# Kernel optimization log

Hardware: AMD Instinct MI355X
Metric: run time of the kernel (lower is better)

## Reference

```python
import jax, jax.numpy as jnp
import numpy as np

RUNS, WAYS, SHOT, QUERIES, D = 512, 5, 5, 15, 640
NS, QS = WAYS * SHOT, WAYS * QUERIES
LAM, ALPHA, UPDATE_RATE, EPOCHS = 10.0, 0.7, 0.6, 3
OT_EPS, OT_MAXITERS = 1e-3, 1000


def compute_entropy(P):
    # P: (runs, n, ways); normalized entropy per row
    P = P + 1e-12
    P = P / P.sum(axis=2, keepdims=True)
    H = -jnp.sum(P * jnp.log(P), axis=2)
    return H / jnp.log(jnp.asarray(P.shape[2], P.dtype))


def sq_cdist(a, b):
    # squared euclidean distance, (runs,n,d) x (runs,m,d) -> (runs,n,m)
    d2 = (a * a).sum(-1)[:, :, None] + (b * b).sum(-1)[:, None, :] \
         - 2.0 * jnp.einsum('bnd,bmd->bnm', a, b)
    return jnp.maximum(d2, 0.0)


def get_distance(f1, f2):
    return jnp.exp(-LAM * sq_cdist(f1, f2))


def build_graph(W):
    n = W.shape[1]
    W = W * (1.0 - jnp.eye(n, dtype=W.dtype)[None])  # zero diagonal
    Dm = W.sum(-1) ** -0.5                            # D^{-1/2}
    return Dm[:, None, :] * W * Dm[:, :, None]


def sinkhorn(M, n_l, labels, eps):
    # faithful port of compute_optimal_transport (class_balance=True)
    nr, n, ways = M.shape
    r = jnp.ones((nr, n), M.dtype)
    c = jnp.full((nr, ways), float(n // ways), M.dtype)  # ones*n//ways (floor)
    onehot = jax.nn.one_hot(labels[:, :n_l], ways, dtype=M.dtype) if n_l > 0 else None

    def cond(st):
        P, u, it = st
        return (jnp.max(jnp.abs(u - P.sum(2))) > eps) & (it <= OT_MAXITERS)

    def body(st):
        P, u, it = st
        u = P.sum(2)
        P = P * (r / u)[:, :, None]
        P = P * (c / P.sum(1))[:, None, :]
        if n_l > 0:
            P = P.at[:, :n_l, :].set(onehot)  # fill_(0) + scatter_(2, labels, 1)
        return P, u, it + 1

    P, _, _ = jax.lax.while_loop(cond, body, (M, jnp.zeros((nr, n), M.dtype), jnp.int32(1)))
    return P


def get_prob(features, proto, ys):
    d2 = sq_cdist(features, proto)
    Pq = jnp.exp(-LAM * d2[:, NS:])
    Pq = sinkhorn(Pq, 0, ys, 1e-3)
    Ps = jax.nn.one_hot(ys, WAYS, dtype=d2.dtype)  # scatter on support rows
    return jnp.concatenate([Ps, Pq], axis=1)


def _forward(xs, xq, ys, yq):
    features = jnp.concatenate([xs, xq], axis=1)           # (runs, ns+qs, d)
    labels = jnp.concatenate([ys, yq], axis=1)
    runs = features.shape[0]
    proto = features[:, :NS].reshape(runs, WAYS, SHOT, -1).mean(axis=2)
    Z = None
    for _ in range(EPOCHS):  # (pre-loop Z / Inverse_W in torch code are dead code)
        features = features[:, :NS + QS]
        Z = get_prob(features, proto, ys)
        ent = compute_entropy(Z)
        Z = Z * (1.0 - ent[..., None])
        # update_prototype
        new_proto = jnp.einsum('bnk,bnd->bkd', Z, features) / Z.sum(axis=1)[..., None]
        proto = (1.0 - UPDATE_RATE) * proto + UPDATE_RATE * new_proto
        dist_proto = get_distance(proto, proto)
        score = compute_entropy(dist_proto)
        omega = ent.mean(axis=1, keepdims=True)
        mask = (score < omega).astype(Z.dtype)             # (runs, ways)
        add_proto = proto * mask[..., None]
        dist_proto = dist_proto * mask[..., None]
        features = jnp.concatenate([features, add_proto], axis=1)  # (runs, ns+qs+ways, d)
        Z = jnp.concatenate([Z, dist_proto], axis=1)
        dist = get_distance(features, features)
        W = build_graph(dist)
        n = features.shape[1]
        Inv = jnp.linalg.inv(jnp.eye(n, dtype=W.dtype)[None] - ALPHA * W)
        Z = Inv @ Z                                         # (I - aW)^{-1} diffusion
        Z = sinkhorn(Z, NS, ys, OT_EPS)
    olabels = jnp.argmax(Z[:, :NS + QS], axis=2)
    matches = (labels == olabels).astype(jnp.float32)
    return matches[:, NS:].mean(axis=1)                     # acc_test: (runs,)


def setup_inputs() -> dict:
    key = jax.random.key(0)
    k1, k2, k3 = jax.random.split(key, 3)
    scale = 0.04  # keeps exp(-lam*dist^2) in fp32 normal range
    xs = scale * jax.random.normal(k1, (RUNS, NS, D), dtype=jnp.float32)
    xq = scale * jax.random.normal(k2, (RUNS, QS, D), dtype=jnp.float32)
    # support labels must be class-block ordered (proto reshape assumes it)
    ys = jnp.tile(jnp.repeat(jnp.arange(WAYS, dtype=jnp.int32), SHOT)[None, :], (RUNS, 1))
    yq = jax.random.randint(k3, (RUNS, QS), 0, WAYS, dtype=jnp.int32)
    return {'xs': xs, 'xq': xq, 'ys': ys, 'yq': yq}


def reference(xs, xq, ys, yq):
    return _forward(xs, xq, ys, yq)
```

## Files before the change

### kernel.cpp

```cpp
#include <hip/hip_runtime.h>
#include <math.h>

#define RUNS  512
#define WAYS  5
#define SHOT  5
#define NSUP  25
#define NQ    75
#define N0    100
#define NF    105
#define DIM   640
#define LAMB  10.0f
#define ALF   0.7f
#define UPD   0.6f
#define OT_EPSF 0.001f
#define OT_MAXIT 1000

#define NTILE 14
#define FCH_ROWS 112
#define FCH_STRIDE 36
#define HALF 56
#define CHUNK 64

#define W_WAKE(g)  ((g) * 16)
#define W_C1(g)    (1024 + (g) * 16)
#define W_C2(s)    (2048 + (s) * 16)
#define W_C0       2176
#define W_SLOT(b,g) (2304 + ((b) * 16 + (g)) * 16)

struct __align__(16) Smem {
  float fch[FCH_ROWS * FCH_STRIDE];
  float pbuf[WAYS * DIM];
  float rowk[112];
  float colk[112];
  float Zm[NF * WAYS];
  float ent[NF];
  float fnorm[112];
  float dm[112];
  float rsumh[112];
  float dp[WAYS * WAYS];
  float pn[WAYS];
  float maskv[WAYS];
  float red[4];
  float pivotv;
  int foundsh;
  int ysl[NSUP];
};
static_assert(sizeof(Smem) <= 40 * 1024, "LDS: 2 blocks/CU (80KB of 160KB)");

__device__ __forceinline__ float wsum(float v) {
#pragma unroll
  for (int o = 32; o > 0; o >>= 1) v += __shfl_xor(v, o, 64);
  return v;
}
__device__ __forceinline__ float wmaxr(float v) {
#pragma unroll
  for (int o = 32; o > 0; o >>= 1) v = fmaxf(v, __shfl_xor(v, o, 64));
  return v;
}
__device__ __forceinline__ float bsum(float v, float* red, int tid) {
  v = wsum(v);
  __syncthreads();
  if ((tid & 63) == 0) red[tid >> 6] = v;
  __syncthreads();
  return (red[0] + red[1]) + (red[2] + red[3]);
}

__device__ __forceinline__ void gbar_found(Smem& sm, unsigned* ctl, unsigned& bi,
                                           int tid, int r, int buf, int base) {
  __syncthreads();
  if (tid == 0) {
    const unsigned tgt = 8u * bi + 7u;
    const unsigned seq = bi + 1u;
    int found = -1;
    bool isroot = false;
    unsigned a = __hip_atomic_fetch_add(&ctl[W_C1(r >> 3)], 1u,
                                        __ATOMIC_RELEASE, __HIP_MEMORY_SCOPE_AGENT);
    if (a == tgt) {
      unsigned b = __hip_atomic_fetch_add(&ctl[W_C2(r >> 6)], 1u,
                                          __ATOMIC_RELEASE, __HIP_MEMORY_SCOPE_AGENT);
      if (b == tgt) {
        unsigned c = __hip_atomic_fetch_add(&ctl[W_C0], 1u,
                                            __ATOMIC_RELEASE, __HIP_MEMORY_SCOPE_AGENT);
        if (c == tgt) isroot = true;
      }
    }
    if (isroot) {
      unsigned long long m = 0ull;
#pragma unroll
      for (int g = 0; g < 16; g++)
        m |= __hip_atomic_load((unsigned long long*)(ctl + W_SLOT(buf, g)),
                               __ATOMIC_RELAXED, __HIP_MEMORY_SCOPE_AGENT);
      for (int p = 0; p < CHUNK; p++) {
        int k = base + p + 1;
        bool cond = (((m >> p) & 1ull) != 0ull) && (k <= OT_MAXIT);
        if (!cond) { found = p; break; }
      }
#pragma unroll
      for (int g = 0; g < 16; g++)
        __hip_atomic_store((unsigned long long*)(ctl + W_SLOT(buf, g)), 0ull,
                           __ATOMIC_RELAXED, __HIP_MEMORY_SCOPE_AGENT);
      unsigned pk = seq | ((unsigned)(found + 1) << 16);
      __hip_atomic_store(&ctl[W_WAKE(0)], pk, __ATOMIC_RELEASE, __HIP_MEMORY_SCOPE_AGENT);
#pragma unroll 4
      for (int g = 1; g < 64; g++)
        __hip_atomic_store(&ctl[W_WAKE(g)], pk, __ATOMIC_RELAXED, __HIP_MEMORY_SCOPE_AGENT);
    } else {
      unsigned w;
      for (;;) {
        w = __hip_atomic_load(&ctl[W_WAKE(r >> 3)], __ATOMIC_RELAXED, __HIP_MEMORY_SCOPE_AGENT);
        if ((w & 0xffffu) >= seq) break;
        __builtin_amdgcn_s_sleep(8);
      }
      found = (int)((w >> 16) & 0xffu) - 1;
    }
    sm.foundsh = found;
    bi++;
  }
  __syncthreads();
}

__device__ __forceinline__ float entropy5(const float* z) {
  float p[5]; float t = 0.f;
#pragma unroll
  for (int w = 0; w < 5; w++) { p[w] = z[w] + 1e-12f; t += p[w]; }
  float H = 0.f;
#pragma unroll
  for (int w = 0; w < 5; w++) { float q = p[w] / t; H -= q * logf(q); }
  return H / logf(5.0f);
}

__device__ __forceinline__ float loadF(const float* xs, const float* xq, int r, int i, int d) {
  return (i < NSUP) ? xs[(r * NSUP + i) * DIM + d] : xq[(r * NQ + (i - NSUP)) * DIM + d];
}

__device__ void sinkhorn_wave(Smem& sm, unsigned* ctl,
                              unsigned& bi, int rowOff, int n, float cval,
                              bool clampLab, int tid, int r, int& sidx) {
  const int lane = tid & 63;
  const int wv = tid >> 6;
  float p0[5], p1[5], u0 = 0.f, u1 = 0.f;
  float q0[5], q1[5], v0 = 0.f, v1 = 0.f;
  bool e0 = false, e1 = false;
  int row0 = 0, y0 = -1;
  if (wv == 0) {
    row0 = lane;
    int row1 = lane + 64;
    e0 = row0 < n; e1 = row1 < n;
    y0 = (clampLab && row0 < NSUP) ? sm.ysl[row0] : -1;
#pragma unroll
    for (int w = 0; w < 5; w++) {
      p0[w] = e0 ? sm.Zm[(rowOff + row0) * 5 + w] : 0.f;
      p1[w] = e1 ? sm.Zm[(rowOff + row1) * 5 + w] : 0.f;
    }
  }
  auto body = [&]() {
    float t0 = 0.f, t1 = 0.f;
#pragma unroll
    for (int w = 0; w < 5; w++) { t0 += p0[w]; t1 += p1[w]; }
    u0 = t0; u1 = t1;
    float i0 = e0 ? 1.0f / t0 : 0.f;
    float i1 = e1 ? 1.0f / t1 : 0.f;
#pragma unroll
    for (int w = 0; w < 5; w++) { p0[w] *= i0; p1[w] *= i1; }
#pragma unroll
    for (int w = 0; w < 5; w++) {
      float cs = wsum(p0[w] + p1[w]);
      float f = cval / cs;
      p0[w] *= f; p1[w] *= f;
    }
    if (y0 >= 0) {
#pragma unroll
      for (int w = 0; w < 5; w++) p0[w] = (y0 == w) ? 1.0f : 0.0f;
    }
  };

  int base = 0;
  while (true) {
    unsigned long long mask = 0ull;
    if (wv == 0) {
#pragma unroll
      for (int w = 0; w < 5; w++) { q0[w] = p0[w]; q1[w] = p1[w]; }
      v0 = u0; v1 = u1;
#pragma unroll 1
      for (int p = 0; p < CHUNK; p++) {
        float t0 = 0.f, t1 = 0.f;
#pragma unroll
        for (int w = 0; w < 5; w++) { t0 += p0[w]; t1 += p1[w]; }
        float res = fmaxf(e0 ? fabsf(u0 - t0) : 0.f, e1 ? fabsf(u1 - t1) : 0.f);
        res = wmaxr(res);
        if (res > OT_EPSF) mask |= (1ull << p);
        body();
      }
      if (lane == 0)
        __hip_atomic_fetch_or((unsigned long long*)(ctl + W_SLOT(sidx & 1, r >> 5)), mask,
                              __ATOMIC_RELAXED, __HIP_MEMORY_SCOPE_AGENT);
    }
    gbar_found(sm, ctl, bi, tid, r, sidx & 1, base);
    int found = sm.foundsh;
    sidx++;
    if (found >= 0) {
      if (wv == 0) {
#pragma unroll
        for (int w = 0; w < 5; w++) { p0[w] = q0[w]; p1[w] = q1[w]; }
        u0 = v0; u1 = v1;
#pragma unroll 1
        for (int p = 0; p < found; p++) body();
#pragma unroll
        for (int w = 0; w < 5; w++) {
          if (e0) sm.Zm[(rowOff + row0) * 5 + w] = p0[w];
          if (e1) sm.Zm[(rowOff + lane + 64) * 5 + w] = p1[w];
        }
      }
      __syncthreads();
      return;
    }
    base += CHUNK;
  }
}

__global__ void init_kernel(unsigned* __restrict__ ctl, float* __restrict__ out) {
  int i = blockIdx.x * blockDim.x + threadIdx.x;
  if (i < 4096) __hip_atomic_store(&ctl[i], 0u, __ATOMIC_RELAXED, __HIP_MEMORY_SCOPE_AGENT);
  if (i < RUNS) out[i] = -1.0f;
}

__global__ __launch_bounds__(256, 2) void fsl_kernel(
    const float* __restrict__ xs, const float* __restrict__ xq,
    const int* __restrict__ ys, const int* __restrict__ yq,
    float* __restrict__ out, unsigned* __restrict__ ctl) {
  __shared__ Smem sm;
  const int tid = threadIdx.x;
  const int r = blockIdx.x;
  const int lane = tid & 63, wid = tid >> 6;
  unsigned bi = 0;
  int sidx = 0;

  for (int i = wid; i < N0; i += 4) {
    float p = 0.f;
    for (int d = lane; d < DIM; d += 64) { float v = loadF(xs, xq, r, i, d); p += v * v; }
    p = wsum(p);
    if (lane == 0) sm.fnorm[i] = p;
  }
  if (tid < NSUP) sm.ysl[tid] = ys[r * NSUP + tid];
  for (int idx = tid; idx < WAYS * DIM; idx += 256) {
    int w = idx / DIM, d = idx % DIM;
    float sacc = 0.f;
#pragma unroll
    for (int s5 = 0; s5 < SHOT; s5++) sacc += xs[(r * NSUP + w * SHOT + s5) * DIM + d];
    sm.pbuf[idx] = sacc / 5.0f;
  }
  __syncthreads();

  int ti = 0, tj = 0;
  if (tid < 210) {
    int t = tid >> 1;
    while (t >= NTILE - ti) { t -= NTILE - ti; ti++; }
    tj = ti + t;
  }
  const int hcol = tid & 1;
  const bool own = tid < 210;
  const int erow = own ? (tid % 105) : 0;
  const int hh = own ? (tid / 105) : 0;
  const int jbase = HALF * hh;

  float (*band)[112] = (float (*)[112])sm.fch;

  for (int ep = 0; ep < 3; ep++) {
    for (int w = wid; w < WAYS; w += 4) {
      float p = 0.f;
      for (int d = lane; d < DIM; d += 64) { float v = sm.pbuf[w * DIM + d]; p += v * v; }
      p = wsum(p);
      if (lane == 0) sm.pn[w] = p;
    }
    __syncthreads();
    for (int pq = wid; pq < NQ * WAYS; pq += 4) {
      int q = pq / 5, w = pq % 5;
      float dt = 0.f;
      for (int d = lane; d < DIM; d += 64)
        dt += xq[(r * NQ + q) * DIM + d] * sm.pbuf[w * DIM + d];
      dt = wsum(dt);
      if (lane == 0) {
        float d2 = fmaxf(sm.fnorm[NSUP + q] + sm.pn[w] - 2.0f * dt, 0.0f);
        sm.Zm[(NSUP + q) * 5 + w] = expf(-LAMB * d2);
      }
    }
    __syncthreads();
    sinkhorn_wave(sm, ctl, bi, NSUP, NQ, 15.0f, false, tid, r, sidx);
    if (tid < NSUP * 5) { int i = tid / 5, w = tid % 5; sm.Zm[i * 5 + w] = (sm.ysl[i] == w) ? 1.0f : 0.0f; }
    __syncthreads();
    if (tid < N0) {
      float e = entropy5(&sm.Zm[tid * 5]);
      sm.ent[tid] = e;
      float f1 = 1.0f - e;
#pragma unroll
      for (int w = 0; w < 5; w++) sm.Zm[tid * 5 + w] *= f1;
    }
    __syncthreads();
    float zs[5];
#pragma unroll
    for (int w = 0; w < 5; w++) zs[w] = bsum(tid < N0 ? sm.Zm[tid * 5 + w] : 0.f, sm.red, tid);
    for (int d = tid; d < DIM; d += 256) {
      float a[5] = {0.f, 0.f, 0.f, 0.f, 0.f};
      for (int i = 0; i < N0; i++) {
        float v = loadF(xs, xq, r, i, d);
#pragma unroll
        for (int w = 0; w < 5; w++) a[w] += sm.Zm[i * 5 + w] * v;
      }
#pragma unroll
      for (int w = 0; w < 5; w++) {
        float old = sm.pbuf[w * DIM + d];
        sm.pbuf[w * DIM + d] = (1.0f - UPD) * old + UPD * (a[w] / zs[w]);
      }
    }
    __syncthreads();
    for (int w = wid; w < WAYS; w += 4) {
      float p = 0.f;
      for (int d = lane; d < DIM; d += 64) { float v = sm.pbuf[w * DIM + d]; p += v * v; }
      p = wsum(p);
      if (lane == 0) sm.pn[w] = p;
    }
    __syncthreads();
    for (int pp5 = wid; pp5 < 25; pp5 += 4) {
      int a5 = pp5 / 5, b5 = pp5 % 5;
      float dt = 0.f;
      for (int d = lane; d < DIM; d += 64)
        dt += sm.pbuf[a5 * DIM + d] * sm.pbuf[b5 * DIM + d];
      dt = wsum(dt);
      if (lane == 0) {
        float d2 = fmaxf(sm.pn[a5] + sm.pn[b5] - 2.0f * dt, 0.0f);
        sm.dp[pp5] = expf(-LAMB * d2);
      }
    }
    __syncthreads();
    float omega = bsum(tid < N0 ? sm.ent[tid] : 0.f, sm.red, tid) / 100.0f;
    if (tid < WAYS) {
      float sc = entropy5(&sm.dp[tid * 5]);
      sm.maskv[tid] = (sc < omega) ? 1.0f : 0.0f;
    }
    __syncthreads();
    if (tid < WAYS) sm.fnorm[N0 + tid] = sm.maskv[tid] * sm.pn[tid];
    if (tid < 25) { int a5 = tid / 5, b5 = tid % 5; sm.Zm[(N0 + a5) * 5 + b5] = sm.dp[tid] * sm.maskv[a5]; }
    __syncthreads();
    float acc[32];
#pragma unroll
    for (int z = 0; z < 32; z++) acc[z] = 0.f;
    for (int c = 0; c < 20; c++) {
      for (int idx = tid; idx < FCH_ROWS * 32; idx += 256) {
        int i = idx >> 5, dc = idx & 31;
        float v = 0.f;
        int d = c * 32 + dc;
        if (i < N0) v = loadF(xs, xq, r, i, d);
        else if (i < NF) v = sm.maskv[i - N0] * sm.pbuf[(i - N0) * DIM + d];
        int gg = dc >> 2, rm = dc & 3;
        sm.fch[i * FCH_STRIDE + (((gg ^ ((i >> 3) & 7)) << 2) | rm)] = v;
      }
      __syncthreads();
      if (tid < 210) {
        int i0 = ti * 8, j0 = tj * 8 + 4 * hcol, si = ti & 7, sj = tj & 7;
#pragma unroll
        for (int g = 0; g < 8; g++) {
          float4 a4[8], b4[4];
#pragma unroll
          for (int rr = 0; rr < 8; rr++)
            a4[rr] = *(const float4*)&sm.fch[(i0 + rr) * FCH_STRIDE + ((g ^ si) << 2)];
#pragma unroll
          for (int cc = 0; cc < 4; cc++)
            b4[cc] = *(const float4*)&sm.fch[(j0 + cc) * FCH_STRIDE + ((g ^ sj) << 2)];
#pragma unroll
          for (int rr = 0; rr < 8; rr++)
#pragma unroll
            for (int cc = 0; cc < 4; cc++)
              acc[rr * 4 + cc] += a4[rr].x * b4[cc].x + a4[rr].y * b4[cc].y +
                                  a4[rr].z * b4[cc].z + a4[rr].w * b4[cc].w;
        }
      }
      __syncthreads();
    }
    float Areg[HALF];
    float rsum = 0.f;
    for (int b = 0; b < NTILE; b++) {
      if (tid < 210) {
        if (ti == b) {
#pragma unroll
          for (int rr = 0; rr < 8; rr++)
#pragma unroll
            for (int cc = 0; cc < 4; cc++)
              band[rr][8 * tj + 4 * hcol + cc] = acc[rr * 4 + cc];
        }
        if (tj == b && ti != b) {
#pragma unroll
          for (int rr = 0; rr < 8; rr++)
#pragma unroll
            for (int cc = 0; cc < 4; cc++)
              band[4 * hcol + cc][8 * ti + rr] = acc[rr * 4 + cc];
        }
      }
      __syncthreads();
      if (own && (erow >> 3) == b) {
        int lr = erow & 7;
#pragma unroll
        for (int jj = 0; jj < HALF; jj++) {
          int j = jbase + jj;
          float wv = 0.f;
          if (j < NF && j != erow) {
            float d2 = fmaxf(sm.fnorm[erow] + sm.fnorm[j] - 2.0f * band[lr][j], 0.0f);
            wv = expf(-LAMB * d2);
          }
          Areg[jj] = wv;
          rsum += wv;
        }
      }
      __syncthreads();
    }
    if (own && hh == 1) sm.rsumh[erow] = rsum;
    __syncthreads();
    if (own && hh == 0) sm.dm[erow] = 1.0f / sqrtf(rsum + sm.rsumh[erow]);
    __syncthreads();
    float cnext = 0.f;
    if (own) {
      float dme = sm.dm[erow];
#pragma unroll
      for (int jj = 0; jj < HALF; jj++) {
        int j = jbase + jj;
        float t = (j < NF) ? (sm.dm[j] * Areg[jj]) * dme : 0.f;
        Areg[jj] = ((j == erow) ? 1.0f : 0.0f) - ALF * t;
      }
      if (hh == 0) cnext = Areg[0];
    }
    if (tid < 112) sm.rowk[tid] = 0.f;
    __syncthreads();
    for (int k = 0; k < NF; k++) {
      int hk = (k < HALF) ? 0 : 1;
      if (own && hh == hk) {
        if (erow == k) { sm.pivotv = cnext; sm.colk[k] = 0.f; }
        else sm.colk[erow] = cnext;
      }
      __syncthreads();
      float pinv = 1.0f / sm.pivotv;
      if (own && erow == k) {
#pragma unroll
        for (int jj = 0; jj < HALF; jj++) {
          int j = jbase + jj;
          if (j > k && j < NF) { Areg[jj] *= pinv; sm.rowk[j] = Areg[jj]; }
        }
        if (hh == hk) sm.rowk[k] = 0.f;
        if (hh == 0) {
#pragma unroll
          for (int w = 0; w < 5; w++) sm.Zm[k * 5 + w] *= pinv;
        }
      }
      __syncthreads();
      if (own) {
        float m = sm.colk[erow];
#pragma unroll
        for (int jj = 0; jj < HALF; jj += 4) {
          float4 rk = *(const float4*)&sm.rowk[jbase + jj];
          Areg[jj + 0] -= m * rk.x;
          Areg[jj + 1] -= m * rk.y;
          Areg[jj + 2] -= m * rk.z;
          Areg[jj + 3] -= m * rk.w;
        }
#pragma unroll
        for (int jj = 0; jj < HALF; jj++)
          if (jbase + jj == k + 1) cnext = Areg[jj];
        if (hh == 0 && erow != k) {
#pragma unroll
          for (int w = 0; w < 5; w++) sm.Zm[erow * 5 + w] -= m * sm.Zm[k * 5 + w];
        }
      }
      __syncthreads();
    }
    sinkhorn_wave(sm, ctl, bi, 0, NF, 21.0f, true, tid, r, sidx);
  }

  float mt = 0.f;
  if (tid < NQ) {
    int row = NSUP + tid;
    float best = sm.Zm[row * 5]; int bl = 0;
#pragma unroll
    for (int w = 1; w < 5; w++) { float v = sm.Zm[row * 5 + w]; if (v > best) { best = v; bl = w; } }
    mt = (yq[r * NQ + tid] == bl) ? 1.0f : 0.0f;
  }
  float tot = bsum(mt, sm.red, tid);
  if (tid == 0) out[r] = tot / 75.0f;
}

extern "C" void kernel_launch(void* const* d_in, const int* in_sizes, int n_in,
                              void* d_out, int out_size, void* d_ws, size_t ws_size,
                              hipStream_t stream) {
  const float* xs = (const float*)d_in[0];
  const float* xq = (const float*)d_in[1];
  const int* ys = (const int*)d_in[2];
  const int* yq = (const int*)d_in[3];
  float* out = (float*)d_out;
  unsigned* ctl = (unsigned*)d_ws;
  init_kernel<<<dim3(16), dim3(256), 0, stream>>>(ctl, out);
  fsl_kernel<<<dim3(RUNS), dim3(256), 0, stream>>>(xs, xq, ys, yq, out, ctl);
}
```

Before: 7.256 ms.

## Remap Sinkhorn rows onto 16-lane groups with DPP row reductions

The Sinkhorn solver previously spread rows across a full 64-lane wave, two rows per lane, and reduced with 6-step cross-lane shuffles. It now gives each lane S rows strided by 16 and does column sums and the residual max with 4 DPP row operations inside a 16-lane group. This shortens the per-iteration reduction chain but raises register work per lane. The pre-chunk snapshot moves from registers to LDS to free registers. The four 16-lane groups compute redundantly and only group 0 writes results.

Result: faster. 6.864 ms (-5.4%).

```diff
diff --git a/kernel.cpp b/kernel.cpp
--- a/kernel.cpp
+++ b/kernel.cpp
@@ -41,6 +41,7 @@
   float pn[WAYS];
   float maskv[WAYS];
   float red[4];
+  float snap[16][44];
   float pivotv;
   int foundsh;
   int ysl[NSUP];
@@ -50,11 +51,6 @@
 __device__ __forceinline__ float wsum(float v) {
 #pragma unroll
   for (int o = 32; o > 0; o >>= 1) v += __shfl_xor(v, o, 64);
-  return v;
-}
-__device__ __forceinline__ float wmaxr(float v) {
-#pragma unroll
-  for (int o = 32; o > 0; o >>= 1) v = fmaxf(v, __shfl_xor(v, o, 64));
   return v;
 }
 __device__ __forceinline__ float bsum(float v, float* red, int tid) {
@@ -63,6 +59,28 @@
   if ((tid & 63) == 0) red[tid >> 6] = v;
   __syncthreads();
   return (red[0] + red[1]) + (red[2] + red[3]);
+}
+
+template <int CTRL>
+__device__ __forceinline__ float dppx(float v) {
+  union U { float f; int i; } a, b;
+  a.f = v;
+  b.i = __builtin_amdgcn_update_dpp(0, a.i, CTRL, 0xF, 0xF, true);
+  return b.f;
+}
+__device__ __forceinline__ float rsum16(float v) {
+  v += dppx<0xB1>(v);
+  v += dppx<0x4E>(v);
+  v += dppx<0x141>(v);
+  v += dppx<0x140>(v);
+  return v;
+}
+__device__ __forceinline__ float rmax16(float v) {
+  v = fmaxf(v, dppx<0xB1>(v));
+  v = fmaxf(v, dppx<0x4E>(v));
+  v = fmaxf(v, dppx<0x141>(v));
+  v = fmaxf(v, dppx<0x140>(v));
+  return v;
 }
 
 __device__ __forceinline__ void gbar_found(Smem& sm, unsigned* ctl, unsigned& bi,
@@ -133,63 +151,83 @@
   return (i < NSUP) ? xs[(r * NSUP + i) * DIM + d] : xq[(r * NQ + (i - NSUP)) * DIM + d];
 }
 
-__device__ void sinkhorn_wave(Smem& sm, unsigned* ctl,
-                              unsigned& bi, int rowOff, int n, float cval,
-                              bool clampLab, int tid, int r, int& sidx) {
+template <int S, bool CLAMP>
+__device__ void sinkhorn_dpp(Smem& sm, unsigned* ctl, unsigned& bi, int rowOff,
+                             int n, float cval, int tid, int r, int& sidx) {
   const int lane = tid & 63;
   const int wv = tid >> 6;
-  float p0[5], p1[5], u0 = 0.f, u1 = 0.f;
-  float q0[5], q1[5], v0 = 0.f, v1 = 0.f;
-  bool e0 = false, e1 = false;
-  int row0 = 0, y0 = -1;
+  const int l16 = lane & 15;
+  const bool grp0 = lane < 16;
+  float p[S][5], u[S];
+  int yv[S];
+  bool val[S];
   if (wv == 0) {
-    row0 = lane;
-    int row1 = lane + 64;
-    e0 = row0 < n; e1 = row1 < n;
-    y0 = (clampLab && row0 < NSUP) ? sm.ysl[row0] : -1;
+#pragma unroll
+    for (int k = 0; k < S; k++) {
+      int rr = 16 * k + l16;
+      val[k] = rr < n;
+#pragma unroll
+      for (int w = 0; w < 5; w++)
+        p[k][w] = val[k] ? sm.Zm[(rowOff + rr) * 5 + w] : 0.f;
+      u[k] = 0.f;
+      yv[k] = (CLAMP && rr < NSUP) ? sm.ysl[rr < NSUP ? rr : 0] : -1;
+    }
+  }
+
+  auto body = [&]() -> float {
+    float res = 0.f;
+#pragma unroll
+    for (int k = 0; k < S; k++) {
+      float t = p[k][0];
+#pragma unroll
+      for (int w = 1; w < 5; w++) t += p[k][w];
+      res = fmaxf(res, val[k] ? fabsf(u[k] - t) : 0.f);
+      u[k] = t;
+      float i0 = val[k] ? 1.0f / t : 0.f;
+#pragma unroll
+      for (int w = 0; w < 5; w++) p[k][w] *= i0;
+    }
+    res = rmax16(res);
 #pragma unroll
     for (int w = 0; w < 5; w++) {
-      p0[w] = e0 ? sm.Zm[(rowOff + row0) * 5 + w] : 0.f;
-      p1[w] = e1 ? sm.Zm[(rowOff + row1) * 5 + w] : 0.f;
-    }
-  }
-  auto body = [&]() {
-    float t0 = 0.f, t1 = 0.f;
-#pragma unroll
-    for (int w = 0; w < 5; w++) { t0 += p0[w]; t1 += p1[w]; }
-    u0 = t0; u1 = t1;
-    float i0 = e0 ? 1.0f / t0 : 0.f;
-    float i1 = e1 ? 1.0f / t1 : 0.f;
-#pragma unroll
-    for (int w = 0; w < 5; w++) { p0[w] *= i0; p1[w] *= i1; }
-#pragma unroll
-    for (int w = 0; w < 5; w++) {
-      float cs = wsum(p0[w] + p1[w]);
+      float cs = p[0][w];
+#pragma unroll
+      for (int k = 1; k < S; k++) cs += p[k][w];
+      cs = rsum16(cs);
       float f = cval / cs;
-      p0[w] *= f; p1[w] *= f;
-    }
-    if (y0 >= 0) {
-#pragma unroll
-      for (int w = 0; w < 5; w++) p0[w] = (y0 == w) ? 1.0f : 0.0f;
-    }
+#pragma unroll
+      for (int k = 0; k < S; k++) p[k][w] *= f;
+    }
+    if (CLAMP) {
+#pragma unroll
+      for (int k = 0; k < S; k++) {
+        if (16 * k < NSUP) {
+          if (yv[k] >= 0) {
+#pragma unroll
+            for (int w = 0; w < 5; w++) p[k][w] = (yv[k] == w) ? 1.0f : 0.0f;
+          }
+        }
+      }
+    }
+    return res;
   };
 
   int base = 0;
   while (true) {
     unsigned long long mask = 0ull;
     if (wv == 0) {
-#pragma unroll
-      for (int w = 0; w < 5; w++) { q0[w] = p0[w]; q1[w] = p1[w]; }
-      v0 = u0; v1 = u1;
+      if (grp0) {
+#pragma unroll
+        for (int k = 0; k < S; k++) {
+#pragma unroll
+          for (int w = 0; w < 5; w++) sm.snap[l16][k * 5 + w] = p[k][w];
+          sm.snap[l16][35 + k] = u[k];
+        }
+      }
 #pragma unroll 1
-      for (int p = 0; p < CHUNK; p++) {
-        float t0 = 0.f, t1 = 0.f;
-#pragma unroll
-        for (int w = 0; w < 5; w++) { t0 += p0[w]; t1 += p1[w]; }
-        float res = fmaxf(e0 ? fabsf(u0 - t0) : 0.f, e1 ? fabsf(u1 - t1) : 0.f);
-        res = wmaxr(res);
-        if (res > OT_EPSF) mask |= (1ull << p);
-        body();
+      for (int pp = 0; pp < CHUNK; pp++) {
+        float res = body();
+        if (res > OT_EPSF) mask |= (1ull << pp);
       }
       if (lane == 0)
         __hip_atomic_fetch_or((unsigned long long*)(ctl + W_SLOT(sidx & 1, r >> 5)), mask,
@@ -201,14 +239,23 @@
     if (found >= 0) {
       if (wv == 0) {
 #pragma unroll
-        for (int w = 0; w < 5; w++) { p0[w] = q0[w]; p1[w] = q1[w]; }
-        u0 = v0; u1 = v1;
+        for (int k = 0; k < S; k++) {
+#pragma unroll
+          for (int w = 0; w < 5; w++) p[k][w] = sm.snap[l16][k * 5 + w];
+          u[k] = sm.snap[l16][35 + k];
+        }
 #pragma unroll 1
-        for (int p = 0; p < found; p++) body();
-#pragma unroll
-        for (int w = 0; w < 5; w++) {
-          if (e0) sm.Zm[(rowOff + row0) * 5 + w] = p0[w];
-          if (e1) sm.Zm[(rowOff + lane + 64) * 5 + w] = p1[w];
+        for (int pp = 0; pp < found; pp++) (void)body();
+        if (grp0) {
+#pragma unroll
+          for (int k = 0; k < S; k++) {
+            if (val[k]) {
+              int rr = 16 * k + l16;
+#pragma unroll
+              for (int w = 0; w < 5; w++)
+                sm.Zm[(rowOff + rr) * 5 + w] = p[k][w];
+            }
+          }
         }
       }
       __syncthreads();
@@ -285,7 +332,7 @@
       }
     }
     __syncthreads();
-    sinkhorn_wave(sm, ctl, bi, NSUP, NQ, 15.0f, false, tid, r, sidx);
+    sinkhorn_dpp<5, false>(sm, ctl, bi, NSUP, NQ, 15.0f, tid, r, sidx);
     if (tid < NSUP * 5) { int i = tid / 5, w = tid % 5; sm.Zm[i * 5 + w] = (sm.ysl[i] == w) ? 1.0f : 0.0f; }
     __syncthreads();
     if (tid < N0) {
@@ -470,7 +517,7 @@
       }
       __syncthreads();
     }
-    sinkhorn_wave(sm, ctl, bi, 0, NF, 21.0f, true, tid, r, sidx);
+    sinkhorn_dpp<7, true>(sm, ctl, bi, 0, NF, 21.0f, tid, r, sidx);
   }
 
   float mt = 0.f;
```
